# Optimization experiments

Measured on AMD Instinct MI355X. Metric: run time of the kernel, lower is better.

The kernel has to match this reference:

```python
import jax, jax.numpy as jnp
import numpy as np

B = 1024
IN = 512      # in_features
O = 64        # out_features
E = 8         # ensamble
K = O * E     # total tiny MLPs, index k = i*E + j (i: output, j: ensemble)


def setup_inputs() -> dict:
    key = jax.random.key(0)
    k1, k2, k3, k4, k5 = jax.random.split(key, 5)
    s = 1.0 / np.sqrt(IN)
    X = jax.random.normal(k1, (B, IN), dtype=jnp.float32)
    # Stacked weights for all K = O*E tiny MLPs.
    # nn.Linear(in,in): y = x @ W1^T + b1, W1: [in_out, in_in]
    W1 = jax.random.uniform(k2, (K, IN, IN), jnp.float32, -s, s)
    b1 = jax.random.uniform(k3, (K, IN), jnp.float32, -s, s)
    # nn.Linear(in,1): W2 squeezed to [K, IN], b2 to [K]
    W2 = jax.random.uniform(k4, (K, IN), jnp.float32, -s, s)
    b2 = jax.random.uniform(k5, (K,), jnp.float32, -s, s)
    return {"X": X, "W1": W1, "b1": b1, "W2": W2, "b2": b2}


def reference(X, W1, b1, W2, b2):
    # h[b,k,:] = relu(X[b] @ W1[k].T + b1[k])  -- one batched GEMM
    h = jax.nn.relu(jnp.einsum('bi,kji->bkj', X, W1) + b1)  # [B,K,IN]
    out = jnp.einsum('bkj,kj->bk', h, W2) + b2              # [B,K]
    # original: concat over ensemble (dim=-1) then stack over out_features (dim=-1)
    out = out.reshape(X.shape[0], O, E).transpose(0, 2, 1)  # [B,E,O]
    return out
```

## Files before the change

kernel.cpp:

```cpp
#include <hip/hip_runtime.h>
#include <hip/hip_bf16.h>

typedef __attribute__((ext_vector_type(8))) short short8;
typedef __attribute__((ext_vector_type(4))) float f32x4;

__device__ __forceinline__ short8 pack8(const f32x4& a, const f32x4& b) {
    union { __hip_bfloat162 h[4]; short8 s; } u;
    u.h[0] = __float22bfloat162_rn(make_float2(a[0], a[1]));
    u.h[1] = __float22bfloat162_rn(make_float2(a[2], a[3]));
    u.h[2] = __float22bfloat162_rn(make_float2(b[0], b[1]));
    u.h[3] = __float22bfloat162_rn(make_float2(b[2], b[3]));
    return u.s;
}

__device__ __forceinline__ int swz4(int g) { return g ^ (((g >> 4) & 3) << 1); }

#define GLDS(GP, LP)                                                          \
    __builtin_amdgcn_global_load_lds(                                         \
        (__attribute__((address_space(1))) void*)(void*)(GP),                 \
        (__attribute__((address_space(3))) void*)(void*)(LP), 16, 0, 0)

__global__ __launch_bounds__(256)
void ens_cvt(const float* __restrict__ X, const float* __restrict__ W1,
             short* __restrict__ WS)
{
    const int t = threadIdx.x, lane = t & 63, wv = t >> 6;
    const int g = blockIdx.x * 4 + wv;
    const int row16 = lane & 15, koct = lane >> 4;
    const float* src;
    short* dst;
    if (blockIdx.x < 4096) {
        const int km = g >> 5, f = g & 31;
        src = W1 + (size_t)km * 262144 + (size_t)(f * 16 + row16) * 512 + koct * 8;
        dst = WS + (size_t)km * 262144 + (size_t)(f * 16) * 512 + lane * 8;
    } else {
        const int mf = g - 16384;
        src = X + (size_t)(mf * 16 + row16) * 512 + koct * 8;
        dst = WS + 134217728ull + (size_t)(mf * 16) * 512 + lane * 8;
    }
#pragma unroll
    for (int ks = 0; ks < 16; ++ks) {
        f32x4 a = *(const f32x4*)(src + ks * 32);
        f32x4 b = *(const f32x4*)(src + ks * 32 + 4);
        *(short8*)(dst + ks * 512) = pack8(a, b);
    }
}

#define ISSUE(H)                                                              \
  do {                                                                        \
    char* sb_ = smem + ((H) & 3) * 32768;                                     \
    GLDS(g0 + (H) * 512, sb_ + (size_t)(s0 + 0) * 1024);                      \
    GLDS(g1 + (H) * 512, sb_ + (size_t)(s0 + 1) * 1024);                      \
    GLDS(g2 + (H) * 512, sb_ + (size_t)(s0 + 2) * 1024);                      \
    GLDS(g3 + (H) * 512, sb_ + (size_t)(s0 + 3) * 1024);                      \
  } while (0)

#define KK(H)                                                                 \
  do {                                                                        \
    const char* rb_ = smem + ((H) & 3) * 32768;                               \
    _Pragma("unroll") for (int mi = 0; mi < 8; ++mi)                          \
        av[mi] = *(const short8*)(rb_ + (wm * 8 + mi) * 1024 + (lane << 4));  \
    _Pragma("unroll") for (int pp = 0; pp < 4; ++pp)                          \
        bv[pp] = *(const short8*)(rb_ + 16384 +                               \
                                  (wn * 4 + pp) * 1024 + (lane << 4));        \
    __builtin_amdgcn_s_setprio(1);                                            \
    _Pragma("unroll") for (int mi = 0; mi < 8; ++mi)                          \
        _Pragma("unroll") for (int pp = 0; pp < 4; ++pp)                      \
            acc[mi][pp] = __builtin_amdgcn_mfma_f32_16x16x32_bf16(            \
                av[mi], bv[pp], acc[mi][pp], 0, 0, 0);                        \
    __builtin_amdgcn_s_setprio(0);                                            \
  } while (0)

__global__ __launch_bounds__(512, 2)
void ens_gemm_dma(const short* __restrict__ Xb, const short* __restrict__ W1b,
                  const float* __restrict__ B1, const float* __restrict__ W2,
                  const float* __restrict__ B2, float* __restrict__ out)
{
    extern __shared__ char smem[];
    const int t    = threadIdx.x;
    const int lane = t & 63;
    const int wv   = t >> 6;
    const int wm   = wv >> 2;
    const int wn   = wv & 3;

    const int bb  = blockIdx.x;
    const int xcd = bb & 7;
    const int j   = bb >> 3;
    const int km  = xcd * 64 + (j >> 3);
    const int sub = j & 7;
    const int mt  = sub >> 1;
    const int nt  = sub & 1;

    const int s0 = wv * 4;
    const short* g0;
    const short* g1;
    const short* g2;
    const short* g3;
    {
        auto gsrc = [&](int s) -> const short* {
            if (s < 16)
                return Xb + (size_t)(mt * 16 + s) * 16 * 512 + lane * 8;
            return W1b + (size_t)km * 262144 +
                   (size_t)(nt * 16 + (s - 16)) * 16 * 512 + lane * 8;
        };
        g0 = gsrc(s0); g1 = gsrc(s0 + 1); g2 = gsrc(s0 + 2); g3 = gsrc(s0 + 3);
    }

    f32x4 acc[8][4];
#pragma unroll
    for (int i = 0; i < 8; ++i)
#pragma unroll
        for (int p = 0; p < 4; ++p)
            acc[i][p] = (f32x4)0.0f;

    short8 av[8], bv[4];

    ISSUE(0);
    ISSUE(1);
    ISSUE(2);
    asm volatile("s_waitcnt vmcnt(8)" ::: "memory");
    __builtin_amdgcn_sched_barrier(0);
    __builtin_amdgcn_s_barrier();
    __builtin_amdgcn_sched_barrier(0);

#pragma unroll 1
    for (int h = 0; h < 16; ++h) {
        if (h < 13) ISSUE(h + 3);
        KK(h);
        if (h < 13)       asm volatile("s_waitcnt vmcnt(8)" ::: "memory");
        else if (h == 13) asm volatile("s_waitcnt vmcnt(4)" ::: "memory");
        else if (h == 14) asm volatile("s_waitcnt vmcnt(0)" ::: "memory");
        if (h < 15) {
            __builtin_amdgcn_sched_barrier(0);
            __builtin_amdgcn_s_barrier();
            __builtin_amdgcn_sched_barrier(0);
        }
    }

    const int nc = lane & 15;
    const int kq = lane >> 4;
    float b1v[4], w2v[4];
#pragma unroll
    for (int pp = 0; pp < 4; ++pp) {
        int n = nt * 256 + (wn * 4 + pp) * 16 + nc;
        b1v[pp] = B1[km * 512 + n];
        w2v[pp] = W2[km * 512 + n];
    }

    float* lout = (float*)smem;
#pragma unroll
    for (int i = 0; i < 8; ++i) {
#pragma unroll
        for (int r = 0; r < 4; ++r) {
            float s = 0.f;
#pragma unroll
            for (int pp = 0; pp < 4; ++pp) {
                float h = acc[i][pp][r] + b1v[pp];
                h = h > 0.f ? h : 0.f;
                s += h * w2v[pp];
            }
#pragma unroll
            for (int d = 1; d < 16; d <<= 1)
                s += __shfl_xor(s, d, 64);
            if (nc == 0) {
                int row = wm * 128 + i * 16 + kq * 4 + r;
                lout[row * 4 + wn] = s;
            }
        }
    }
    __syncthreads();
    if (t < 256) {
        float s = lout[t * 4 + 0] + lout[t * 4 + 1] + lout[t * 4 + 2] + lout[t * 4 + 3];
        if (nt == 0) s += B2[km];
        int b = mt * 256 + t;
        atomicAdd(out + (size_t)b * 512 + (km & 7) * 64 + (km >> 3), s);
    }
}

#define FISSUE(S, BASE, KT1)                                                  \
  do {                                                                        \
    const float* q_ = (BASE) + (KT1) * 64;                                    \
    S[0] = *(const f32x4*)q_;          S[1] = *(const f32x4*)(q_ + 4);        \
    S[2] = *(const f32x4*)(q_ + 32);   S[3] = *(const f32x4*)(q_ + 36);       \
    const float* q2_ = q_ + 65536;                                            \
    S[4] = *(const f32x4*)q2_;         S[5] = *(const f32x4*)(q2_ + 4);       \
    S[6] = *(const f32x4*)(q2_ + 32);  S[7] = *(const f32x4*)(q2_ + 36);      \
  } while (0)

#define FWRITEB(S, WB, OPOFF)                                                 \
  do {                                                                        \
    char* d0_ = (WB) + (OPOFF) + wfrag;                                       \
    *(short8*)d0_ = pack8(S[0], S[1]);                                        \
    *(short8*)(d0_ + 1024) = pack8(S[2], S[3]);                               \
    char* d1_ = d0_ + 16384;                                                  \
    *(short8*)d1_ = pack8(S[4], S[5]);                                        \
    *(short8*)(d1_ + 1024) = pack8(S[6], S[7]);                               \
  } while (0)

#define FKK(RB, KKV)                                                          \
  do {                                                                        \
    _Pragma("unroll") for (int mi = 0; mi < 8; ++mi)                          \
        av[mi] = *(const short8*)((RB) +                                      \
            (((wm * 8 + mi) * 2 + (KKV)) << 10) + rdo);                       \
    _Pragma("unroll") for (int pp = 0; pp < 4; ++pp)                          \
        bv[pp] = *(const short8*)((RB) + 32768 +                              \
            (((wn * 4 + pp) * 2 + (KKV)) << 10) + rdo);                       \
    __builtin_amdgcn_s_setprio(1);                                            \
    _Pragma("unroll") for (int mi = 0; mi < 8; ++mi)                          \
        _Pragma("unroll") for (int pp = 0; pp < 4; ++pp)                      \
            acc[mi][pp] = __builtin_amdgcn_mfma_f32_16x16x32_bf16(            \
                av[mi], bv[pp], acc[mi][pp], 0, 0, 0);                        \
    __builtin_amdgcn_s_setprio(0);                                            \
  } while (0)

#define FPRO_WRITE(TT, ROFF)                                                  \
  do {                                                                        \
    short8 a_ = pack8(TT[0], TT[1]);                                          \
    short8 b_ = pack8(TT[2], TT[3]);                                          \
    char* d_ = smem + (ROFF) + wfrag;                                         \
    *(short8*)d_ = a_;                                                        \
    *(short8*)(d_ + 1024) = b_;                                               \
  } while (0)

__global__ __launch_bounds__(512, 2)
void ens_mlp_fallback(const float* __restrict__ X,
                      const float* __restrict__ W1,
                      const float* __restrict__ B1,
                      const float* __restrict__ W2,
                      const float* __restrict__ B2,
                      float* __restrict__ out)
{
    extern __shared__ char smem[];
    const int t    = threadIdx.x;
    const int lane = t & 63;
    const int wv   = t >> 6;
    const int wm   = wv >> 2;
    const int wn   = wv & 3;

    const int bb  = blockIdx.x;
    const int xcd = bb & 7;
    const int j   = bb >> 3;
    const int km  = xcd * 64 + (j >> 3);
    const int sub = j & 7;
    const int mt  = sub >> 1;
    const int nt  = sub & 1;

    const float* __restrict__ W1k = W1 + (size_t)km * (512 * 512);

    const int lr = t >> 2;
    const int c  = t & 3;
    const float* As = X   + (size_t)(mt * 256 + lr) * 512 + c * 8;
    const float* Bs = W1k + (size_t)(nt * 256 + lr) * 512 + c * 8;
    const int wfrag = ((lr >> 4) << 11) + (swz4((c << 4) | (lr & 15)) << 4);
    const int rdo   = swz4(lane) << 4;

    {
        f32x4 t0[4], t1[4], t2[4], t3[4];
        const float* q;
        q = As;          t0[0]=*(const f32x4*)q; t0[1]=*(const f32x4*)(q+4); t0[2]=*(const f32x4*)(q+32); t0[3]=*(const f32x4*)(q+36);
        q = As + 65536;  t1[0]=*(const f32x4*)q; t1[1]=*(const f32x4*)(q+4); t1[2]=*(const f32x4*)(q+32); t1[3]=*(const f32x4*)(q+36);
        q = Bs;          t2[0]=*(const f32x4*)q; t2[1]=*(const f32x4*)(q+4); t2[2]=*(const f32x4*)(q+32); t2[3]=*(const f32x4*)(q+36);
        q = Bs + 65536;  t3[0]=*(const f32x4*)q; t3[1]=*(const f32x4*)(q+4); t3[2]=*(const f32x4*)(q+32); t3[3]=*(const f32x4*)(q+36);
        asm volatile("s_waitcnt vmcnt(12)" ::: "memory"); FPRO_WRITE(t0, 0);
        asm volatile("s_waitcnt vmcnt(8)"  ::: "memory"); FPRO_WRITE(t1, 16384);
        asm volatile("s_waitcnt vmcnt(4)"  ::: "memory"); FPRO_WRITE(t2, 32768);
        asm volatile("s_waitcnt vmcnt(0)"  ::: "memory"); FPRO_WRITE(t3, 49152);
        asm volatile("s_waitcnt lgkmcnt(0)" ::: "memory");
        __builtin_amdgcn_sched_barrier(0);
        __builtin_amdgcn_s_barrier();
    }

    f32x4 acc[8][4];
#pragma unroll
    for (int i = 0; i < 8; ++i)
#pragma unroll
        for (int p = 0; p < 4; ++p)
            acc[i][p] = (f32x4)0.0f;

    short8 av[8], bv[4];
    f32x4 sS[8];

#pragma unroll 1
    for (int kt = 0; kt < 7; ++kt) {
        const char* rb = smem + (kt & 1) * 65536;
        char* wb       = smem + ((kt + 1) & 1) * 65536;

        FISSUE(sS, Bs, kt + 1);
        FKK(rb, 0);
        asm volatile("s_waitcnt vmcnt(0)" ::: "memory");
        FWRITEB(sS, wb, 32768);
        FISSUE(sS, As, kt + 1);
        FKK(rb, 1);
        asm volatile("s_waitcnt vmcnt(0)" ::: "memory");
        FWRITEB(sS, wb, 0);
        asm volatile("s_waitcnt lgkmcnt(0)" ::: "memory");
        __builtin_amdgcn_sched_barrier(0);
        __builtin_amdgcn_s_barrier();
    }
    {
        const char* rb = smem + 65536;
        FKK(rb, 0);
        FKK(rb, 1);
    }

    const int nc = lane & 15;
    const int kq = lane >> 4;
    float b1v[4], w2v[4];
#pragma unroll
    for (int pp = 0; pp < 4; ++pp) {
        int n = nt * 256 + (wn * 4 + pp) * 16 + nc;
        b1v[pp] = B1[km * 512 + n];
        w2v[pp] = W2[km * 512 + n];
    }

    float* lout = (float*)smem;
#pragma unroll
    for (int i = 0; i < 8; ++i) {
#pragma unroll
        for (int r = 0; r < 4; ++r) {
            float s = 0.f;
#pragma unroll
            for (int pp = 0; pp < 4; ++pp) {
                float h = acc[i][pp][r] + b1v[pp];
                h = h > 0.f ? h : 0.f;
                s += h * w2v[pp];
            }
#pragma unroll
            for (int d = 1; d < 16; d <<= 1)
                s += __shfl_xor(s, d, 64);
            if (nc == 0) {
                int row = wm * 128 + i * 16 + kq * 4 + r;
                lout[row * 4 + wn] = s;
            }
        }
    }
    __syncthreads();
    if (t < 256) {
        float s = lout[t * 4 + 0] + lout[t * 4 + 1] + lout[t * 4 + 2] + lout[t * 4 + 3];
        if (nt == 0) s += B2[km];
        int b = mt * 256 + t;
        atomicAdd(out + (size_t)b * 512 + (km & 7) * 64 + (km >> 3), s);
    }
}

extern "C" void kernel_launch(void* const* d_in, const int* in_sizes, int n_in,
                              void* d_out, int out_size, void* d_ws, size_t ws_size,
                              hipStream_t stream) {
    const float* X  = (const float*)d_in[0];
    const float* W1 = (const float*)d_in[1];
    const float* B1 = (const float*)d_in[2];
    const float* W2 = (const float*)d_in[3];
    const float* B2 = (const float*)d_in[4];
    float* out = (float*)d_out;

    hipMemsetAsync(out, 0, (size_t)out_size * sizeof(float), stream);

    const size_t NEED = 269484032ull;
    if (ws_size >= NEED) {
        short* WS = (short*)d_ws;
        ens_cvt<<<dim3(4112), dim3(256), 0, stream>>>(X, W1, WS);
        ens_gemm_dma<<<dim3(4096), dim3(512), 131072, stream>>>(
            WS + 134217728ull, WS, B1, W2, B2, out);
    } else {
        ens_mlp_fallback<<<dim3(4096), dim3(512), 131072, stream>>>(
            X, W1, B1, W2, B2, out);
    }
}
```

Before: 470.2 us.

## Restructure GEMM main loop into double-buffered 64-K tiles with four-phase ping-pong

Replaces the four-stage ring of 32-wide K slices with two 64 KiB buffers, each holding a 64-wide K tile. Each tile is split into four phases (M-half by K-half), and the global-to-LDS loads for the next tile are interleaved into the first two phases. Barriers now bracket every phase, in a ping-pong schedule meant to overlap LDS reads, DMA issue and MFMA and to halve A-register usage. In exchange it adds more barriers per tile and only two-deep buffering, which shortens the prefetch distance.

```diff
diff --git a/kernel.cpp b/kernel.cpp
--- a/kernel.cpp
+++ b/kernel.cpp
@@ -46,29 +46,35 @@
     }
 }
 
-#define ISSUE(H)                                                              \
-  do {                                                                        \
-    char* sb_ = smem + ((H) & 3) * 32768;                                     \
-    GLDS(g0 + (H) * 512, sb_ + (size_t)(s0 + 0) * 1024);                      \
-    GLDS(g1 + (H) * 512, sb_ + (size_t)(s0 + 1) * 1024);                      \
-    GLDS(g2 + (H) * 512, sb_ + (size_t)(s0 + 2) * 1024);                      \
-    GLDS(g3 + (H) * 512, sb_ + (size_t)(s0 + 3) * 1024);                      \
-  } while (0)
-
-#define KK(H)                                                                 \
-  do {                                                                        \
-    const char* rb_ = smem + ((H) & 3) * 32768;                               \
-    _Pragma("unroll") for (int mi = 0; mi < 8; ++mi)                          \
-        av[mi] = *(const short8*)(rb_ + (wm * 8 + mi) * 1024 + (lane << 4));  \
-    _Pragma("unroll") for (int pp = 0; pp < 4; ++pp)                          \
-        bv[pp] = *(const short8*)(rb_ + 16384 +                               \
-                                  (wn * 4 + pp) * 1024 + (lane << 4));        \
+#define PH(MH, KK, DOI, DOVM)                                                 \
+  do {                                                                        \
+    _Pragma("unroll") for (int ii = 0; ii < 4; ++ii)                          \
+        av[ii] = *(const short8*)(rb +                                        \
+            (((wm * 8 + (MH) * 4 + ii) * 2 + (KK)) << 10) + l16);             \
+    if ((MH) == 0) {                                                          \
+      _Pragma("unroll") for (int pp = 0; pp < 4; ++pp)                        \
+          bv[pp] = *(const short8*)(rb + 32768 +                              \
+              (((wn * 4 + pp) * 2 + (KK)) << 10) + l16);                      \
+    }                                                                         \
+    if ((DOI) == 1) {                                                         \
+      GLDS(g0 + koff, wb + d0); GLDS(g1 + koff, wb + d1);                     \
+      GLDS(g2 + koff, wb + d2); GLDS(g3 + koff, wb + d3);                     \
+    } else if ((DOI) == 2) {                                                  \
+      GLDS(g4 + koff, wb + d4); GLDS(g5 + koff, wb + d5);                     \
+      GLDS(g6 + koff, wb + d6); GLDS(g7 + koff, wb + d7);                     \
+    }                                                                         \
+    __builtin_amdgcn_s_barrier();                                             \
+    asm volatile("s_waitcnt lgkmcnt(0)" ::: "memory");                        \
+    __builtin_amdgcn_sched_barrier(0);                                        \
     __builtin_amdgcn_s_setprio(1);                                            \
-    _Pragma("unroll") for (int mi = 0; mi < 8; ++mi)                          \
+    _Pragma("unroll") for (int ii = 0; ii < 4; ++ii)                          \
         _Pragma("unroll") for (int pp = 0; pp < 4; ++pp)                      \
-            acc[mi][pp] = __builtin_amdgcn_mfma_f32_16x16x32_bf16(            \
-                av[mi], bv[pp], acc[mi][pp], 0, 0, 0);                        \
+            acc[(MH) * 4 + ii][pp] = __builtin_amdgcn_mfma_f32_16x16x32_bf16( \
+                av[ii], bv[pp], acc[(MH) * 4 + ii][pp], 0, 0, 0);             \
     __builtin_amdgcn_s_setprio(0);                                            \
+    __builtin_amdgcn_sched_barrier(0);                                        \
+    if (DOVM) asm volatile("s_waitcnt vmcnt(0)" ::: "memory");                \
+    __builtin_amdgcn_s_barrier();                                             \
   } while (0)
 
 __global__ __launch_bounds__(512, 2)
@@ -79,6 +85,7 @@
     extern __shared__ char smem[];
     const int t    = threadIdx.x;
     const int lane = t & 63;
+    const int l16  = lane << 4;
     const int wv   = t >> 6;
     const int wm   = wv >> 2;
     const int wn   = wv & 3;
@@ -91,19 +98,21 @@
     const int mt  = sub >> 1;
     const int nt  = sub & 1;
 
-    const int s0 = wv * 4;
-    const short* g0;
-    const short* g1;
-    const short* g2;
-    const short* g3;
-    {
-        auto gsrc = [&](int s) -> const short* {
-            if (s < 16)
-                return Xb + (size_t)(mt * 16 + s) * 16 * 512 + lane * 8;
-            return W1b + (size_t)km * 262144 +
-                   (size_t)(nt * 16 + (s - 16)) * 16 * 512 + lane * 8;
+    const short* g0; const short* g1; const short* g2; const short* g3;
+    const short* g4; const short* g5; const short* g6; const short* g7;
+    int d0, d1, d2, d3, d4, d5, d6, d7;
+    {
+        auto gsrc = [&](int q, int& d) -> const short* {
+            int g  = wv * 8 + q;
+            int op = g >> 5, ri = (g >> 1) & 15, kk = g & 1;
+            d = op * 32768 + ((ri * 2 + kk) << 10);
+            const short* base = (op == 0)
+                ? Xb + (size_t)(mt * 16 + ri) * 8192
+                : W1b + (size_t)km * 262144 + (size_t)(nt * 16 + ri) * 8192;
+            return base + kk * 512 + lane * 8;
         };
-        g0 = gsrc(s0); g1 = gsrc(s0 + 1); g2 = gsrc(s0 + 2); g3 = gsrc(s0 + 3);
+        g0 = gsrc(0, d0); g1 = gsrc(1, d1); g2 = gsrc(2, d2); g3 = gsrc(3, d3);
+        g4 = gsrc(4, d4); g5 = gsrc(5, d5); g6 = gsrc(6, d6); g7 = gsrc(7, d7);
     }
 
     f32x4 acc[8][4];
@@ -113,28 +122,37 @@
         for (int p = 0; p < 4; ++p)
             acc[i][p] = (f32x4)0.0f;
 
-    short8 av[8], bv[4];
-
-    ISSUE(0);
-    ISSUE(1);
-    ISSUE(2);
-    asm volatile("s_waitcnt vmcnt(8)" ::: "memory");
-    __builtin_amdgcn_sched_barrier(0);
-    __builtin_amdgcn_s_barrier();
-    __builtin_amdgcn_sched_barrier(0);
+    short8 av[4], bv[4];
+
+    {
+        char* wb = smem;
+        GLDS(g0, wb + d0); GLDS(g1, wb + d1); GLDS(g2, wb + d2); GLDS(g3, wb + d3);
+        GLDS(g4, wb + d4); GLDS(g5, wb + d5); GLDS(g6, wb + d6); GLDS(g7, wb + d7);
+        asm volatile("s_waitcnt vmcnt(0)" ::: "memory");
+        __builtin_amdgcn_sched_barrier(0);
+        __builtin_amdgcn_s_barrier();
+    }
 
 #pragma unroll 1
-    for (int h = 0; h < 16; ++h) {
-        if (h < 13) ISSUE(h + 3);
-        KK(h);
-        if (h < 13)       asm volatile("s_waitcnt vmcnt(8)" ::: "memory");
-        else if (h == 13) asm volatile("s_waitcnt vmcnt(4)" ::: "memory");
-        else if (h == 14) asm volatile("s_waitcnt vmcnt(0)" ::: "memory");
-        if (h < 15) {
-            __builtin_amdgcn_sched_barrier(0);
-            __builtin_amdgcn_s_barrier();
-            __builtin_amdgcn_sched_barrier(0);
-        }
+    for (int kt = 0; kt < 7; ++kt) {
+        const char* rb = smem + (kt & 1) * 65536;
+        char* wb       = smem + ((kt + 1) & 1) * 65536;
+        const int koff = (kt + 1) << 10;
+
+        PH(0, 0, 1, 0);
+        PH(1, 0, 2, 0);
+        PH(0, 1, 0, 0);
+        PH(1, 1, 0, 1);
+    }
+    {
+        const char* rb = smem + 65536;
+        char* wb = smem;
+        const int koff = 0;
+        (void)wb; (void)koff;
+        PH(0, 0, 0, 0);
+        PH(1, 0, 0, 0);
+        PH(0, 1, 0, 0);
+        PH(1, 1, 0, 0);
     }
 
     const int nc = lane & 15;
```

Result: no change. 479.2 us (+1.9%).

## Load MFMA fragments directly from global into registers, dropping LDS staging

Applied to the files above, without the earlier changes.

Replaces the LDS ring buffer filled by global_load_lds, along with its per-step block barriers, with per-wave direct global loads of A/B fragments into two register sets that alternate with MFMA. This removes barrier synchronisation and LDS traffic and shrinks shared memory to a small reduction buffer. In exchange, waves sharing a block now each fetch overlapping tiles from global memory, which multiplies L2 traffic and raises register pressure.

```diff
diff --git a/kernel.cpp b/kernel.cpp
--- a/kernel.cpp
+++ b/kernel.cpp
@@ -14,11 +14,6 @@
 }
 
 __device__ __forceinline__ int swz4(int g) { return g ^ (((g >> 4) & 3) << 1); }
-
-#define GLDS(GP, LP)                                                          \
-    __builtin_amdgcn_global_load_lds(                                         \
-        (__attribute__((address_space(1))) void*)(void*)(GP),                 \
-        (__attribute__((address_space(3))) void*)(void*)(LP), 16, 0, 0)
 
 __global__ __launch_bounds__(256)
 void ens_cvt(const float* __restrict__ X, const float* __restrict__ W1,
@@ -46,37 +41,30 @@
     }
 }
 
-#define ISSUE(H)                                                              \
-  do {                                                                        \
-    char* sb_ = smem + ((H) & 3) * 32768;                                     \
-    GLDS(g0 + (H) * 512, sb_ + (size_t)(s0 + 0) * 1024);                      \
-    GLDS(g1 + (H) * 512, sb_ + (size_t)(s0 + 1) * 1024);                      \
-    GLDS(g2 + (H) * 512, sb_ + (size_t)(s0 + 2) * 1024);                      \
-    GLDS(g3 + (H) * 512, sb_ + (size_t)(s0 + 3) * 1024);                      \
-  } while (0)
-
-#define KK(H)                                                                 \
-  do {                                                                        \
-    const char* rb_ = smem + ((H) & 3) * 32768;                               \
+#define LOADSET(AV, BV, POFF)                                                 \
+  do {                                                                        \
     _Pragma("unroll") for (int mi = 0; mi < 8; ++mi)                          \
-        av[mi] = *(const short8*)(rb_ + (wm * 8 + mi) * 1024 + (lane << 4));  \
+        AV[mi] = *(const short8*)(pa + mi * 8192 + (POFF));                   \
     _Pragma("unroll") for (int pp = 0; pp < 4; ++pp)                          \
-        bv[pp] = *(const short8*)(rb_ + 16384 +                               \
-                                  (wn * 4 + pp) * 1024 + (lane << 4));        \
+        BV[pp] = *(const short8*)(pb + pp * 8192 + (POFF));                   \
+  } while (0)
+
+#define MM(AV, BV)                                                            \
+  do {                                                                        \
     __builtin_amdgcn_s_setprio(1);                                            \
     _Pragma("unroll") for (int mi = 0; mi < 8; ++mi)                          \
         _Pragma("unroll") for (int pp = 0; pp < 4; ++pp)                      \
             acc[mi][pp] = __builtin_amdgcn_mfma_f32_16x16x32_bf16(            \
-                av[mi], bv[pp], acc[mi][pp], 0, 0, 0);                        \
+                AV[mi], BV[pp], acc[mi][pp], 0, 0, 0);                        \
     __builtin_amdgcn_s_setprio(0);                                            \
   } while (0)
 
 __global__ __launch_bounds__(512, 2)
-void ens_gemm_dma(const short* __restrict__ Xb, const short* __restrict__ W1b,
-                  const float* __restrict__ B1, const float* __restrict__ W2,
-                  const float* __restrict__ B2, float* __restrict__ out)
+void ens_gemm_direct(const short* __restrict__ Xb, const short* __restrict__ W1b,
+                     const float* __restrict__ B1, const float* __restrict__ W2,
+                     const float* __restrict__ B2, float* __restrict__ out)
 {
-    extern __shared__ char smem[];
+    __shared__ float lout[1024];
     const int t    = threadIdx.x;
     const int lane = t & 63;
     const int wv   = t >> 6;
@@ -91,20 +79,9 @@
     const int mt  = sub >> 1;
     const int nt  = sub & 1;
 
-    const int s0 = wv * 4;
-    const short* g0;
-    const short* g1;
-    const short* g2;
-    const short* g3;
-    {
-        auto gsrc = [&](int s) -> const short* {
-            if (s < 16)
-                return Xb + (size_t)(mt * 16 + s) * 16 * 512 + lane * 8;
-            return W1b + (size_t)km * 262144 +
-                   (size_t)(nt * 16 + (s - 16)) * 16 * 512 + lane * 8;
-        };
-        g0 = gsrc(s0); g1 = gsrc(s0 + 1); g2 = gsrc(s0 + 2); g3 = gsrc(s0 + 3);
-    }
+    const short* pa = Xb + (size_t)(mt * 16 + wm * 8) * 8192 + lane * 8;
+    const short* pb = W1b + (size_t)km * 262144 +
+                      (size_t)(nt * 16 + wn * 4) * 8192 + lane * 8;
 
     f32x4 acc[8][4];
 #pragma unroll
@@ -113,29 +90,22 @@
         for (int p = 0; p < 4; ++p)
             acc[i][p] = (f32x4)0.0f;
 
-    short8 av[8], bv[4];
-
-    ISSUE(0);
-    ISSUE(1);
-    ISSUE(2);
-    asm volatile("s_waitcnt vmcnt(8)" ::: "memory");
-    __builtin_amdgcn_sched_barrier(0);
-    __builtin_amdgcn_s_barrier();
-    __builtin_amdgcn_sched_barrier(0);
+    short8 avP[8], bvP[4], avQ[8], bvQ[4];
+
+    LOADSET(avP, bvP, 0);
+    LOADSET(avQ, bvQ, 512);
+    pa += 1024; pb += 1024;
 
 #pragma unroll 1
-    for (int h = 0; h < 16; ++h) {
-        if (h < 13) ISSUE(h + 3);
-        KK(h);
-        if (h < 13)       asm volatile("s_waitcnt vmcnt(8)" ::: "memory");
-        else if (h == 13) asm volatile("s_waitcnt vmcnt(4)" ::: "memory");
-        else if (h == 14) asm volatile("s_waitcnt vmcnt(0)" ::: "memory");
-        if (h < 15) {
-            __builtin_amdgcn_sched_barrier(0);
-            __builtin_amdgcn_s_barrier();
-            __builtin_amdgcn_sched_barrier(0);
-        }
-    }
+    for (int kt = 0; kt < 7; ++kt) {
+        MM(avP, bvP);
+        LOADSET(avP, bvP, 0);
+        MM(avQ, bvQ);
+        LOADSET(avQ, bvQ, 512);
+        pa += 1024; pb += 1024;
+    }
+    MM(avP, bvP);
+    MM(avQ, bvQ);
 
     const int nc = lane & 15;
     const int kq = lane >> 4;
@@ -147,7 +117,6 @@
         w2v[pp] = W2[km * 512 + n];
     }
 
-    float* lout = (float*)smem;
 #pragma unroll
     for (int i = 0; i < 8; ++i) {
 #pragma unroll
@@ -359,7 +328,7 @@
     if (ws_size >= NEED) {
         short* WS = (short*)d_ws;
         ens_cvt<<<dim3(4112), dim3(256), 0, stream>>>(X, W1, WS);
-        ens_gemm_dma<<<dim3(4096), dim3(512), 131072, stream>>>(
+        ens_gemm_direct<<<dim3(4096), dim3(512), 0, stream>>>(
             WS + 134217728ull, WS, B1, W2, B2, out);
     } else {
         ens_mlp_fallback<<<dim3(4096), dim3(512), 131072, stream>>>(
```

New measurement: 519.6 us. +10.5%, slower.
